# Kernel tuning notes

Measured on AMD Instinct MI355X. Metric: run time of the kernel, lower is better.

Reference implementation:

```python
import jax, jax.numpy as jnp
import numpy as np

N, E = 100000, 3200000
F_IN, HID, NCLS = 1433, 8, 7
H1, H2 = 8, 1
NEG_SLOPE = 0.2


def gat_layer(x, W, att_src, att_dst, bias, src, dst, heads, ch):
    n = x.shape[0]
    h = (x @ W).reshape(n, heads, ch)                      # [N,H,C]
    a_s = (h * att_src).sum(-1)                            # [N,H]
    a_d = (h * att_dst).sum(-1)                            # [N,H]
    e = a_s[src] + a_d[dst]                                # [Etot,H]
    e = jnp.where(e > 0, e, NEG_SLOPE * e)                 # leaky_relu(0.2)
    m = jax.ops.segment_max(e, dst, num_segments=n)        # per-dst max
    e = jnp.exp(e - m[dst])
    denom = jax.ops.segment_sum(e, dst, num_segments=n)
    alpha = e / (denom[dst] + 1e-16)                       # segment softmax
    msg = h[src] * alpha[:, :, None]                       # [Etot,H,C]
    out = jax.ops.segment_sum(msg, dst, num_segments=n)    # [N,H,C]
    return out.mean(axis=1) + bias                         # concat=False -> head mean


def setup_inputs() -> dict:
    key = jax.random.key(0)
    ks = jax.random.split(key, 10)
    x = jax.random.normal(ks[0], (N, F_IN), dtype=jnp.float32)
    edge_index = jax.random.randint(ks[1], (2, E), 0, N, dtype=jnp.int32)
    s = 0.1
    W1 = jax.random.normal(ks[2], (F_IN, H1 * HID), dtype=jnp.float32) * s
    att_src1 = jax.random.normal(ks[3], (H1, HID), dtype=jnp.float32) * s
    att_dst1 = jax.random.normal(ks[4], (H1, HID), dtype=jnp.float32) * s
    b1 = jnp.zeros((HID,), dtype=jnp.float32)
    W2 = jax.random.normal(ks[5], (HID, H2 * NCLS), dtype=jnp.float32) * s
    att_src2 = jax.random.normal(ks[6], (H2, NCLS), dtype=jnp.float32) * s
    att_dst2 = jax.random.normal(ks[7], (H2, NCLS), dtype=jnp.float32) * s
    b2 = jnp.zeros((NCLS,), dtype=jnp.float32)
    return {"x": x, "edge_index": edge_index, "W1": W1, "att_src1": att_src1,
            "att_dst1": att_dst1, "b1": b1, "W2": W2, "att_src2": att_src2,
            "att_dst2": att_dst2, "b2": b2}


def reference(x, edge_index, W1, att_src1, att_dst1, b1, W2, att_src2, att_dst2, b2):
    n = x.shape[0]
    loops = jnp.arange(n, dtype=edge_index.dtype)
    src = jnp.concatenate([edge_index[0], loops])  # PyG add_self_loops=True
    dst = jnp.concatenate([edge_index[1], loops])
    h = jax.nn.elu(gat_layer(x, W1, att_src1, att_dst1, b1, src, dst, H1, HID))
    out = gat_layer(h, W2, att_src2, att_dst2, b2, src, dst, H2, NCLS)
    return jax.nn.log_softmax(out, axis=-1)
```

## Files before the change

### kernel.cpp

```cpp
#include <hip/hip_runtime.h>

#define N_NODES 100000
#define E_EDGES 3200000
#define F_IN    1433
#define K_PAD   1472
#define NCH     98
#define KPH     64

typedef _Float16 f16x4 __attribute__((ext_vector_type(4)));
typedef _Float16 f16x8 __attribute__((ext_vector_type(8)));
typedef float    f32x4 __attribute__((ext_vector_type(4)));

__device__ __forceinline__ void gload_lds16(const void* g, void* l) {
    __builtin_amdgcn_global_load_lds(
        (const __attribute__((address_space(1))) unsigned int*)g,
        (__attribute__((address_space(3))) unsigned int*)l, 16, 0, 0);
}

__global__ void k_init(const float* __restrict__ w1, _Float16* __restrict__ w1t,
                       int* __restrict__ counts) {
    int i = blockIdx.x * 256 + threadIdx.x;
    if (i < N_NODES) counts[i] = 0;
    if (i < 64 * K_PAD) {
        int n = i / K_PAD, k = i - n * K_PAD;
        float v = (k < F_IN) ? w1[(size_t)k * 64 + n] : 0.f;
        w1t[i] = (_Float16)v;
    }
}

__global__ void k_hist(const int* __restrict__ dst, int* __restrict__ counts) {
    int idx = blockIdx.x * 256 + threadIdx.x;
    int4 d4 = ((const int4*)dst)[idx];
    atomicAdd(&counts[d4.x], 1);
    atomicAdd(&counts[d4.y], 1);
    atomicAdd(&counts[d4.z], 1);
    atomicAdd(&counts[d4.w], 1);
}

__global__ void k_scan_a(const int* __restrict__ counts, int* __restrict__ csum) {
    __shared__ int sh[256];
    int b = blockIdx.x, t = threadIdx.x;
    int s = 0;
    for (int j = 0; j < 4; ++j) {
        int idx = b * 1024 + j * 256 + t;
        if (idx < N_NODES) s += counts[idx];
    }
    sh[t] = s; __syncthreads();
    for (int off = 128; off > 0; off >>= 1) {
        if (t < off) sh[t] += sh[t + off];
        __syncthreads();
    }
    if (t == 0) csum[b] = sh[0];
}

__global__ void k_scan_b(int* __restrict__ csum) {
    __shared__ int sh[128];
    int t = threadIdx.x;
    int v = (t < NCH) ? csum[t] : 0;
    sh[t] = v; __syncthreads();
    for (int off = 1; off < 128; off <<= 1) {
        int u = (t >= off) ? sh[t - off] : 0;
        __syncthreads();
        sh[t] += u;
        __syncthreads();
    }
    if (t < NCH) csum[t] = sh[t] - v;
}

__global__ void k_scan_c(const int* __restrict__ counts, const int* __restrict__ csum,
                         int* __restrict__ offsets, int* __restrict__ cursor) {
    __shared__ int sh[256];
    int b = blockIdx.x, t = threadIdx.x;
    int base = b * 1024 + t * 4;
    int c0 = (base + 0 < N_NODES) ? counts[base + 0] : 0;
    int c1 = (base + 1 < N_NODES) ? counts[base + 1] : 0;
    int c2 = (base + 2 < N_NODES) ? counts[base + 2] : 0;
    int c3 = (base + 3 < N_NODES) ? counts[base + 3] : 0;
    int tot = c0 + c1 + c2 + c3;
    sh[t] = tot; __syncthreads();
    for (int off = 1; off < 256; off <<= 1) {
        int v = (t >= off) ? sh[t - off] : 0;
        __syncthreads();
        sh[t] += v;
        __syncthreads();
    }
    int excl = sh[t] - tot;
    int o = csum[b] + excl;
    if (base + 0 < N_NODES) { offsets[base + 0] = o;            cursor[base + 0] = o; }
    if (base + 1 < N_NODES) { int q = o + c0;      offsets[base + 1] = q; cursor[base + 1] = q; }
    if (base + 2 < N_NODES) { int q = o + c0 + c1; offsets[base + 2] = q; cursor[base + 2] = q; }
    if (base + 3 < N_NODES) { int q = o + c0 + c1 + c2; offsets[base + 3] = q; cursor[base + 3] = q; }
}

__global__ __launch_bounds__(256) void k_gemm_scat(const float* __restrict__ x,
                                                   const _Float16* __restrict__ w1t,
                                                   const float* __restrict__ att_src1,
                                                   const float* __restrict__ att_dst1,
                                                   _Float16* __restrict__ h1,
                                                   float* __restrict__ a_s1,
                                                   float* __restrict__ a_d1,
                                                   const int* __restrict__ src,
                                                   const int* __restrict__ dst,
                                                   int* __restrict__ cursor,
                                                   int* __restrict__ sorted_src) {
    __shared__ __align__(16) char AsB[2][64 * 256];
    __shared__ __align__(16) char BsB[2][64 * 128];
    const int tid = threadIdx.x;

    if (blockIdx.x & 1) {
        const int sid = blockIdx.x >> 1;
        for (int sweep = 0; sweep < 7; ++sweep) {
            #pragma unroll
            for (int rep = 0; rep < 2; ++rep) {
                int i4 = sid * 512 + rep * 256 + tid;
                if (i4 < E_EDGES / 4) {
                    int4 s4 = ((const int4*)src)[i4];
                    int4 d4 = ((const int4*)dst)[i4];
                    int p;
                    if ((d4.x >> 14) == sweep) { p = atomicAdd(&cursor[d4.x], 1); sorted_src[p] = s4.x; }
                    if ((d4.y >> 14) == sweep) { p = atomicAdd(&cursor[d4.y], 1); sorted_src[p] = s4.y; }
                    if ((d4.z >> 14) == sweep) { p = atomicAdd(&cursor[d4.z], 1); sorted_src[p] = s4.z; }
                    if ((d4.w >> 14) == sweep) { p = atomicAdd(&cursor[d4.w], 1); sorted_src[p] = s4.w; }
                }
            }
        }
        return;
    }

    const int gid  = blockIdx.x >> 1;
    const int lane = tid & 63;
    const int wave = tid >> 6;
    const int l16  = lane & 15;
    const int l4   = lane >> 4;
    const int brow0 = gid * 64;

    f32x4 acc[4] = {};

    auto stageA = [&](int buf, int ph) {
        #pragma unroll
        for (int j = 0; j < 4; ++j) {
            int p = j * 256 + tid;
            int row = p >> 4, q = p & 15;
            int qs = q ^ (row & 7);
            int grow = brow0 + row; if (grow > N_NODES - 1) grow = N_NODES - 1;
            const float* gp = x + (size_t)grow * F_IN + ph * KPH + qs * 4;
            gload_lds16(gp, AsB[buf] + j * 4096 + wave * 1024);
        }
    };
    auto stageB = [&](int buf, int ph) {
        #pragma unroll
        for (int j = 0; j < 2; ++j) {
            int p = j * 256 + tid;
            int col = p >> 3, c = p & 7;
            int cs = c ^ (col & 7);
            const _Float16* gp = w1t + (size_t)col * K_PAD + ph * KPH + cs * 8;
            gload_lds16(gp, BsB[buf] + j * 4096 + wave * 1024);
        }
    };
    auto stageTailA = [&](int buf) {
        for (int i = tid; i < 1024; i += 256) {
            int row = i >> 4, q = i & 15;
            int qs = q ^ (row & 7);
            int grow = brow0 + row; if (grow > N_NODES - 1) grow = N_NODES - 1;
            const float* gp = x + (size_t)grow * F_IN;
            float4 v;
            #pragma unroll
            for (int jj = 0; jj < 4; ++jj) {
                int k = 1408 + qs * 4 + jj;
                ((float*)&v)[jj] = (k < F_IN) ? gp[k] : 0.f;
            }
            *(float4*)(AsB[buf] + row * 256 + q * 16) = v;
        }
    };
    auto compute = [&](int buf) {
        const int rA = wave * 16 + l16;
        const char* Ab = AsB[buf] + rA * 256;
        const int r7 = rA & 7;
        #pragma unroll
        for (int st = 0; st < 4; ++st) {
            float4 af = *(const float4*)(Ab + ((((st << 2) + l4) ^ r7) << 4));
            f16x4 a = { (_Float16)af.x, (_Float16)af.y, (_Float16)af.z, (_Float16)af.w };
            #pragma unroll
            for (int t = 0; t < 4; ++t) {
                const int cB = t * 16 + l16;
                const int chunk = (st << 1) + (l4 >> 1);
                const int boff = cB * 128 + ((chunk ^ (cB & 7)) << 4) + ((l4 & 1) << 3);
                f16x4 b = *(const f16x4*)(BsB[buf] + boff);
                acc[t] = __builtin_amdgcn_mfma_f32_16x16x16f16(a, b, acc[t], 0, 0, 0);
            }
        }
    };

    stageA(0, 0); stageB(0, 0);
    stageA(1, 1); stageB(1, 1);
    for (int ph = 0; ph <= 20; ++ph) {
        asm volatile("s_waitcnt vmcnt(6)" ::: "memory");
        __builtin_amdgcn_sched_barrier(0);
        __builtin_amdgcn_s_barrier();
        compute(ph & 1);
        asm volatile("s_waitcnt lgkmcnt(0)" ::: "memory");
        __builtin_amdgcn_s_barrier();
        int nxt = ph + 2;
        if (nxt < 22)       { stageA(ph & 1, nxt); stageB(ph & 1, nxt); }
        else if (nxt == 22) { stageTailA(ph & 1);  stageB(ph & 1, 22);  }
    }
    asm volatile("s_waitcnt vmcnt(0) lgkmcnt(0)" ::: "memory");
    __builtin_amdgcn_sched_barrier(0);
    __builtin_amdgcn_s_barrier();
    compute(1);
    compute(0);

    const int wrow0 = brow0 + wave * 16;
    #pragma unroll
    for (int t = 0; t < 4; ++t) {
        const int head = t * 2 + (l16 >> 3);
        const int ch   = l16 & 7;
        const float asc = att_src1[head * 8 + ch];
        const float adc = att_dst1[head * 8 + ch];
        #pragma unroll
        for (int j = 0; j < 4; ++j) {
            int r = wrow0 + l4 * 4 + j;
            float ps = acc[t][j] * asc, pd = acc[t][j] * adc;
            ps += __shfl_xor(ps, 1); ps += __shfl_xor(ps, 2); ps += __shfl_xor(ps, 4);
            pd += __shfl_xor(pd, 1); pd += __shfl_xor(pd, 2); pd += __shfl_xor(pd, 4);
            if (r < N_NODES) {
                h1[(size_t)r * 64 + t * 16 + l16] = (_Float16)acc[t][j];
                if (ch == 0) {
                    a_s1[r * 8 + head] = ps;
                    a_d1[r * 8 + head] = pd;
                }
            }
        }
    }
}

__global__ __launch_bounds__(256) void k_agg1(
    const int* __restrict__ offsets, const int* __restrict__ counts,
    const int* __restrict__ sorted_src,
    const float* __restrict__ a_s1, const float* __restrict__ a_d1,
    const _Float16* __restrict__ h1, const float* __restrict__ b1,
    const float* __restrict__ w2, const float* __restrict__ att_src2,
    const float* __restrict__ att_dst2,
    _Float16* __restrict__ g, float* __restrict__ a_s2, float* __restrict__ a_d2) {
    const int lane = threadIdx.x & 63;
    const int wave = threadIdx.x >> 6;
    const int h    = lane & 7;
    const int es   = lane >> 3;
    const int n    = blockIdx.x * 4 + wave;
    const int start = offsets[n];
    const int cnt   = counts[n];
    const float adn = a_d1[n * 8 + h];
    float et = a_s1[n * 8 + h] + adn;
    const float e_self = et > 0.f ? et : 0.2f * et;

    float m = e_self, denom = 0.f;
    float acc[8] = {0.f,0.f,0.f,0.f,0.f,0.f,0.f,0.f};
    if (es == 0) {
        denom = 1.f;
        f16x8 hv0 = *(const f16x8*)(h1 + (size_t)n * 64 + h * 8);
        #pragma unroll
        for (int c = 0; c < 8; ++c) acc[c] = (float)hv0[c];
    }
    for (int i = es; i < cnt; i += 32) {
        const int i1 = i + 8, i2 = i + 16, i3 = i + 24;
        const bool b1v = i1 < cnt, b2v = i2 < cnt, b3v = i3 < cnt;
        int s0 = sorted_src[start + i];
        int s1 = sorted_src[start + (b1v ? i1 : i)];
        int s2 = sorted_src[start + (b2v ? i2 : i)];
        int s3 = sorted_src[start + (b3v ? i3 : i)];
        float a0 = a_s1[s0 * 8 + h];
        float a1 = a_s1[s1 * 8 + h];
        float a2 = a_s1[s2 * 8 + h];
        float a3 = a_s1[s3 * 8 + h];
        f16x8 v0 = *(const f16x8*)(h1 + (size_t)s0 * 64 + h * 8);
        f16x8 v1 = *(const f16x8*)(h1 + (size_t)s1 * 64 + h * 8);
        f16x8 v2 = *(const f16x8*)(h1 + (size_t)s2 * 64 + h * 8);
        f16x8 v3 = *(const f16x8*)(h1 + (size_t)s3 * 64 + h * 8);
        {
            float e = a0 + adn; e = e > 0.f ? e : 0.2f * e;
            if (e > m + 8.f) { float sc = __expf(m - e); denom *= sc;
                #pragma unroll
                for (int c = 0; c < 8; ++c) acc[c] *= sc; m = e; }
            float p = __expf(e - m); denom += p;
            #pragma unroll
            for (int c = 0; c < 8; ++c) acc[c] += p * (float)v0[c];
        }
        if (b1v) {
            float e = a1 + adn; e = e > 0.f ? e : 0.2f * e;
            if (e > m + 8.f) { float sc = __expf(m - e); denom *= sc;
                #pragma unroll
                for (int c = 0; c < 8; ++c) acc[c] *= sc; m = e; }
            float p = __expf(e - m); denom += p;
            #pragma unroll
            for (int c = 0; c < 8; ++c) acc[c] += p * (float)v1[c];
        }
        if (b2v) {
            float e = a2 + adn; e = e > 0.f ? e : 0.2f * e;
            if (e > m + 8.f) { float sc = __expf(m - e); denom *= sc;
                #pragma unroll
                for (int c = 0; c < 8; ++c) acc[c] *= sc; m = e; }
            float p = __expf(e - m); denom += p;
            #pragma unroll
            for (int c = 0; c < 8; ++c) acc[c] += p * (float)v2[c];
        }
        if (b3v) {
            float e = a3 + adn; e = e > 0.f ? e : 0.2f * e;
            if (e > m + 8.f) { float sc = __expf(m - e); denom *= sc;
                #pragma unroll
                for (int c = 0; c < 8; ++c) acc[c] *= sc; m = e; }
            float p = __expf(e - m); denom += p;
            #pragma unroll
            for (int c = 0; c < 8; ++c) acc[c] += p * (float)v3[c];
        }
    }
    #pragma unroll
    for (int d = 8; d < 64; d <<= 1) {
        float mo = __shfl_xor(m, d);
        float dn = __shfl_xor(denom, d);
        float mn = fmaxf(m, mo);
        float sa = __expf(m - mn), sb = __expf(mo - mn);
        denom = denom * sa + dn * sb;
        #pragma unroll
        for (int c = 0; c < 8; ++c) {
            float ao = __shfl_xor(acc[c], d);
            acc[c] = acc[c] * sa + ao * sb;
        }
        m = mn;
    }
    float inv = 1.f / (denom + 1e-16f);
    float hc[8];
    #pragma unroll
    for (int c = 0; c < 8; ++c) {
        float v = acc[c] * inv;
        v += __shfl_xor(v, 1);
        v += __shfl_xor(v, 2);
        v += __shfl_xor(v, 4);
        float o = 0.125f * v + b1[c];
        hc[c] = o > 0.f ? o : expm1f(o);
    }
    if (lane == 0) {
        float s2 = 0.f, d2 = 0.f;
        f16x8 gr;
        #pragma unroll
        for (int j = 0; j < 7; ++j) {
            float t = 0.f;
            #pragma unroll
            for (int c = 0; c < 8; ++c) t += hc[c] * w2[c * 7 + j];
            gr[j] = (_Float16)t;
            s2 += t * att_src2[j];
            d2 += t * att_dst2[j];
        }
        gr[7] = (_Float16)0.f;
        *(f16x8*)(g + (size_t)n * 8) = gr;
        a_s2[n] = s2;
        a_d2[n] = d2;
    }
}

__global__ __launch_bounds__(256) void k_agg2(
    const int* __restrict__ offsets, const int* __restrict__ counts,
    const int* __restrict__ sorted_src,
    const float* __restrict__ a_s2, const float* __restrict__ a_d2,
    const _Float16* __restrict__ g, const float* __restrict__ b2,
    float* __restrict__ outp) {
    const int tid  = threadIdx.x;
    const int lane = tid & 63;
    const int wave = tid >> 6;
    const int grp  = lane >> 3;
    const int s    = lane & 7;
    const int n    = blockIdx.x * 32 + wave * 8 + grp;
    const int start = offsets[n];
    const int cnt   = counts[n];
    const float adn = a_d2[n];
    float et = a_s2[n] + adn;
    const float e_self = et > 0.f ? et : 0.2f * et;

    float m = e_self, denom = 0.f;
    float acc[8] = {0.f,0.f,0.f,0.f,0.f,0.f,0.f,0.f};
    if (s == 0) {
        denom = 1.f;
        f16x8 gv0 = *(const f16x8*)(g + (size_t)n * 8);
        #pragma unroll
        for (int c = 0; c < 8; ++c) acc[c] = (float)gv0[c];
    }
    for (int i = s; i < cnt; i += 32) {
        const int i1 = i + 8, i2 = i + 16, i3 = i + 24;
        const bool b1v = i1 < cnt, b2v = i2 < cnt, b3v = i3 < cnt;
        int s0 = sorted_src[start + i];
        int s1 = sorted_src[start + (b1v ? i1 : i)];
        int s2 = sorted_src[start + (b2v ? i2 : i)];
        int s3 = sorted_src[start + (b3v ? i3 : i)];
        float a0 = a_s2[s0], a1 = a_s2[s1], a2 = a_s2[s2], a3 = a_s2[s3];
        f16x8 v0 = *(const f16x8*)(g + (size_t)s0 * 8);
        f16x8 v1 = *(const f16x8*)(g + (size_t)s1 * 8);
        f16x8 v2 = *(const f16x8*)(g + (size_t)s2 * 8);
        f16x8 v3 = *(const f16x8*)(g + (size_t)s3 * 8);
        {
            float e = a0 + adn; e = e > 0.f ? e : 0.2f * e;
            if (e > m + 8.f) { float sc = __expf(m - e); denom *= sc;
                #pragma unroll
                for (int c = 0; c < 8; ++c) acc[c] *= sc; m = e; }
            float p = __expf(e - m); denom += p;
            #pragma unroll
            for (int c = 0; c < 8; ++c) acc[c] += p * (float)v0[c];
        }
        if (b1v) {
            float e = a1 + adn; e = e > 0.f ? e : 0.2f * e;
            if (e > m + 8.f) { float sc = __expf(m - e); denom *= sc;
                #pragma unroll
                for (int c = 0; c < 8; ++c) acc[c] *= sc; m = e; }
            float p = __expf(e - m); denom += p;
            #pragma unroll
            for (int c = 0; c < 8; ++c) acc[c] += p * (float)v1[c];
        }
        if (b2v) {
            float e = a2 + adn; e = e > 0.f ? e : 0.2f * e;
            if (e > m + 8.f) { float sc = __expf(m - e); denom *= sc;
                #pragma unroll
                for (int c = 0; c < 8; ++c) acc[c] *= sc; m = e; }
            float p = __expf(e - m); denom += p;
            #pragma unroll
            for (int c = 0; c < 8; ++c) acc[c] += p * (float)v2[c];
        }
        if (b3v) {
            float e = a3 + adn; e = e > 0.f ? e : 0.2f * e;
            if (e > m + 8.f) { float sc = __expf(m - e); denom *= sc;
                #pragma unroll
                for (int c = 0; c < 8; ++c) acc[c] *= sc; m = e; }
            float p = __expf(e - m); denom += p;
            #pragma unroll
            for (int c = 0; c < 8; ++c) acc[c] += p * (float)v3[c];
        }
    }
    #pragma unroll
    for (int d = 1; d < 8; d <<= 1) {
        float mo = __shfl_xor(m, d, 8);
        float dn = __shfl_xor(denom, d, 8);
        float mn = fmaxf(m, mo);
        float sa = __expf(m - mn), sb = __expf(mo - mn);
        denom = denom * sa + dn * sb;
        #pragma unroll
        for (int c = 0; c < 8; ++c) {
            float ao = __shfl_xor(acc[c], d, 8);
            acc[c] = acc[c] * sa + ao * sb;
        }
        m = mn;
    }
    float inv = 1.f / (denom + 1e-16f);
    float o[7]; float mx = -1e30f;
    #pragma unroll
    for (int c = 0; c < 7; ++c) { o[c] = acc[c] * inv + b2[c]; mx = fmaxf(mx, o[c]); }
    float se = 0.f;
    #pragma unroll
    for (int c = 0; c < 7; ++c) se += __expf(o[c] - mx);
    float ls = mx + logf(se);
    if (s < 7) outp[n * 7 + s] = o[s] - ls;
}

extern "C" void kernel_launch(void* const* d_in, const int* in_sizes, int n_in,
                              void* d_out, int out_size, void* d_ws, size_t ws_size,
                              hipStream_t stream) {
    const float* x        = (const float*)d_in[0];
    const int*   ei       = (const int*)d_in[1];
    const float* W1       = (const float*)d_in[2];
    const float* att_src1 = (const float*)d_in[3];
    const float* att_dst1 = (const float*)d_in[4];
    const float* b1       = (const float*)d_in[5];
    const float* W2       = (const float*)d_in[6];
    const float* att_src2 = (const float*)d_in[7];
    const float* att_dst2 = (const float*)d_in[8];
    const float* b2       = (const float*)d_in[9];
    const int* src = ei;
    const int* dst = ei + E_EDGES;

    char* ws = (char*)d_ws;
    size_t off = 0;
    auto alloc = [&](size_t bytes) -> char* {
        char* p = ws + off;
        off = (off + bytes + 255) & ~(size_t)255;
        return p;
    };
    _Float16* h1         = (_Float16*)alloc((size_t)N_NODES * 64 * 2);
    float*    a_s1       = (float*)   alloc((size_t)N_NODES * 8 * 4);
    float*    a_d1       = (float*)   alloc((size_t)N_NODES * 8 * 4);
    _Float16* w1t        = (_Float16*)alloc((size_t)64 * K_PAD * 2);
    int*      counts     = (int*)     alloc((size_t)N_NODES * 4);
    int*      offsets    = (int*)     alloc((size_t)N_NODES * 4);
    int*      cursor     = (int*)     alloc((size_t)N_NODES * 4);
    int*      csum       = (int*)     alloc((size_t)NCH * 4);
    int*      sorted_src = (int*)     alloc((size_t)(E_EDGES + 32) * 4);
    _Float16* gbuf       = (_Float16*)alloc((size_t)N_NODES * 8 * 2);
    float*    a_s2       = (float*)   alloc((size_t)N_NODES * 4);
    float*    a_d2       = (float*)   alloc((size_t)N_NODES * 4);
    float*    outp       = (float*)d_out;

    hipLaunchKernelGGL(k_init,      dim3(391),   dim3(256), 0, stream, W1, w1t, counts);
    hipLaunchKernelGGL(k_hist,      dim3(3125),  dim3(256), 0, stream, dst, counts);
    hipLaunchKernelGGL(k_scan_a,    dim3(NCH),   dim3(256), 0, stream, counts, csum);
    hipLaunchKernelGGL(k_scan_b,    dim3(1),     dim3(128), 0, stream, csum);
    hipLaunchKernelGGL(k_scan_c,    dim3(NCH),   dim3(256), 0, stream, counts, csum, offsets, cursor);
    hipLaunchKernelGGL(k_gemm_scat, dim3(3126),  dim3(256), 0, stream,
                       x, w1t, att_src1, att_dst1, h1, a_s1, a_d1,
                       src, dst, cursor, sorted_src);
    hipLaunchKernelGGL(k_agg1,      dim3(25000), dim3(256), 0, stream, offsets, counts, sorted_src,
                       a_s1, a_d1, h1, b1, W2, att_src2, att_dst2, gbuf, a_s2, a_d2);
    hipLaunchKernelGGL(k_agg2,      dim3(3125),  dim3(256), 0, stream, offsets, counts, sorted_src,
                       a_s2, a_d2, gbuf, b2, outp);
}
```

Measured before the change: 535.1 us.

## Split scatter from GEMM and deepen GEMM pipeline to four K32 stages

The fused GEMM-plus-edge-scatter kernel becomes two separate kernels: a standalone atomic scatter, and a layer-1 GEMM with K tiles of 32 and a four-buffer global-to-LDS pipeline in place of two buffers of 64. Padding K to 1440 lets the special scalar tail-staging path go away. For the last tile, the x loads now run past the end of each row into the next one, which is safe only because the padded weights there are zero. The goal is more loads in flight and a simpler GEMM, at the cost of no longer overlapping the scatter with the GEMM, plus an extra launch.

```diff
diff --git a/kernel.cpp b/kernel.cpp
--- a/kernel.cpp
+++ b/kernel.cpp
@@ -3,9 +3,9 @@
 #define N_NODES 100000
 #define E_EDGES 3200000
 #define F_IN    1433
-#define K_PAD   1472
+#define K_PAD   1440
 #define NCH     98
-#define KPH     64
+#define KPH     32
 
 typedef _Float16 f16x4 __attribute__((ext_vector_type(4)));
 typedef _Float16 f16x8 __attribute__((ext_vector_type(8)));
@@ -92,99 +92,75 @@
     if (base + 3 < N_NODES) { int q = o + c0 + c1 + c2; offsets[base + 3] = q; cursor[base + 3] = q; }
 }
 
-__global__ __launch_bounds__(256) void k_gemm_scat(const float* __restrict__ x,
-                                                   const _Float16* __restrict__ w1t,
-                                                   const float* __restrict__ att_src1,
-                                                   const float* __restrict__ att_dst1,
-                                                   _Float16* __restrict__ h1,
-                                                   float* __restrict__ a_s1,
-                                                   float* __restrict__ a_d1,
-                                                   const int* __restrict__ src,
-                                                   const int* __restrict__ dst,
-                                                   int* __restrict__ cursor,
-                                                   int* __restrict__ sorted_src) {
-    __shared__ __align__(16) char AsB[2][64 * 256];
-    __shared__ __align__(16) char BsB[2][64 * 128];
+__global__ void k_scatter(const int* __restrict__ src, const int* __restrict__ dst,
+                          int* __restrict__ cursor, int* __restrict__ sorted_src) {
     const int tid = threadIdx.x;
-
-    if (blockIdx.x & 1) {
-        const int sid = blockIdx.x >> 1;
-        for (int sweep = 0; sweep < 7; ++sweep) {
-            #pragma unroll
-            for (int rep = 0; rep < 2; ++rep) {
-                int i4 = sid * 512 + rep * 256 + tid;
-                if (i4 < E_EDGES / 4) {
-                    int4 s4 = ((const int4*)src)[i4];
-                    int4 d4 = ((const int4*)dst)[i4];
-                    int p;
-                    if ((d4.x >> 14) == sweep) { p = atomicAdd(&cursor[d4.x], 1); sorted_src[p] = s4.x; }
-                    if ((d4.y >> 14) == sweep) { p = atomicAdd(&cursor[d4.y], 1); sorted_src[p] = s4.y; }
-                    if ((d4.z >> 14) == sweep) { p = atomicAdd(&cursor[d4.z], 1); sorted_src[p] = s4.z; }
-                    if ((d4.w >> 14) == sweep) { p = atomicAdd(&cursor[d4.w], 1); sorted_src[p] = s4.w; }
-                }
+    const int sid = blockIdx.x;
+    for (int sweep = 0; sweep < 7; ++sweep) {
+        #pragma unroll
+        for (int rep = 0; rep < 2; ++rep) {
+            int i4 = sid * 512 + rep * 256 + tid;
+            if (i4 < E_EDGES / 4) {
+                int4 s4 = ((const int4*)src)[i4];
+                int4 d4 = ((const int4*)dst)[i4];
+                int p;
+                if ((d4.x >> 14) == sweep) { p = atomicAdd(&cursor[d4.x], 1); sorted_src[p] = s4.x; }
+                if ((d4.y >> 14) == sweep) { p = atomicAdd(&cursor[d4.y], 1); sorted_src[p] = s4.y; }
+                if ((d4.z >> 14) == sweep) { p = atomicAdd(&cursor[d4.z], 1); sorted_src[p] = s4.z; }
+                if ((d4.w >> 14) == sweep) { p = atomicAdd(&cursor[d4.w], 1); sorted_src[p] = s4.w; }
             }
         }
-        return;
-    }
-
-    const int gid  = blockIdx.x >> 1;
+    }
+}
+
+__global__ __launch_bounds__(256) void k_gemm1(const float* __restrict__ x,
+                                               const _Float16* __restrict__ w1t,
+                                               const float* __restrict__ att_src1,
+                                               const float* __restrict__ att_dst1,
+                                               _Float16* __restrict__ h1,
+                                               float* __restrict__ a_s1,
+                                               float* __restrict__ a_d1) {
+    __shared__ __align__(16) char AsB[4][64 * 128];
+    __shared__ __align__(16) char BsB[4][64 * 64];
+    const int tid  = threadIdx.x;
     const int lane = tid & 63;
     const int wave = tid >> 6;
     const int l16  = lane & 15;
     const int l4   = lane >> 4;
-    const int brow0 = gid * 64;
+    const int brow0 = blockIdx.x * 64;
 
     f32x4 acc[4] = {};
 
     auto stageA = [&](int buf, int ph) {
         #pragma unroll
-        for (int j = 0; j < 4; ++j) {
+        for (int j = 0; j < 2; ++j) {
             int p = j * 256 + tid;
-            int row = p >> 4, q = p & 15;
+            int row = p >> 3, q = p & 7;
             int qs = q ^ (row & 7);
-            int grow = brow0 + row; if (grow > N_NODES - 1) grow = N_NODES - 1;
+            int grow = brow0 + row; if (grow >= N_NODES) grow = 0;
             const float* gp = x + (size_t)grow * F_IN + ph * KPH + qs * 4;
             gload_lds16(gp, AsB[buf] + j * 4096 + wave * 1024);
         }
     };
     auto stageB = [&](int buf, int ph) {
-        #pragma unroll
-        for (int j = 0; j < 2; ++j) {
-            int p = j * 256 + tid;
-            int col = p >> 3, c = p & 7;
-            int cs = c ^ (col & 7);
-            const _Float16* gp = w1t + (size_t)col * K_PAD + ph * KPH + cs * 8;
-            gload_lds16(gp, BsB[buf] + j * 4096 + wave * 1024);
-        }
-    };
-    auto stageTailA = [&](int buf) {
-        for (int i = tid; i < 1024; i += 256) {
-            int row = i >> 4, q = i & 15;
-            int qs = q ^ (row & 7);
-            int grow = brow0 + row; if (grow > N_NODES - 1) grow = N_NODES - 1;
-            const float* gp = x + (size_t)grow * F_IN;
-            float4 v;
-            #pragma unroll
-            for (int jj = 0; jj < 4; ++jj) {
-                int k = 1408 + qs * 4 + jj;
-                ((float*)&v)[jj] = (k < F_IN) ? gp[k] : 0.f;
-            }
-            *(float4*)(AsB[buf] + row * 256 + q * 16) = v;
-        }
+        int col = tid >> 2, c = tid & 3;
+        int cs = c ^ (col & 3);
+        const _Float16* gp = w1t + (size_t)col * K_PAD + ph * KPH + cs * 8;
+        gload_lds16(gp, BsB[buf] + wave * 1024);
     };
     auto compute = [&](int buf) {
         const int rA = wave * 16 + l16;
-        const char* Ab = AsB[buf] + rA * 256;
+        const char* Ab = AsB[buf] + rA * 128;
         const int r7 = rA & 7;
         #pragma unroll
-        for (int st = 0; st < 4; ++st) {
+        for (int st = 0; st < 2; ++st) {
             float4 af = *(const float4*)(Ab + ((((st << 2) + l4) ^ r7) << 4));
             f16x4 a = { (_Float16)af.x, (_Float16)af.y, (_Float16)af.z, (_Float16)af.w };
             #pragma unroll
             for (int t = 0; t < 4; ++t) {
                 const int cB = t * 16 + l16;
                 const int chunk = (st << 1) + (l4 >> 1);
-                const int boff = cB * 128 + ((chunk ^ (cB & 7)) << 4) + ((l4 & 1) << 3);
+                const int boff = cB * 64 + ((chunk ^ (cB & 3)) << 4) + ((l4 & 1) << 3);
                 f16x4 b = *(const f16x4*)(BsB[buf] + boff);
                 acc[t] = __builtin_amdgcn_mfma_f32_16x16x16f16(a, b, acc[t], 0, 0, 0);
             }
@@ -193,22 +169,29 @@
 
     stageA(0, 0); stageB(0, 0);
     stageA(1, 1); stageB(1, 1);
-    for (int ph = 0; ph <= 20; ++ph) {
-        asm volatile("s_waitcnt vmcnt(6)" ::: "memory");
+    stageA(2, 2); stageB(2, 2);
+    stageA(3, 3); stageB(3, 3);
+    for (int ph = 0; ph <= 41; ++ph) {
+        asm volatile("s_waitcnt vmcnt(9)" ::: "memory");
         __builtin_amdgcn_sched_barrier(0);
         __builtin_amdgcn_s_barrier();
-        compute(ph & 1);
+        compute(ph & 3);
         asm volatile("s_waitcnt lgkmcnt(0)" ::: "memory");
         __builtin_amdgcn_s_barrier();
-        int nxt = ph + 2;
-        if (nxt < 22)       { stageA(ph & 1, nxt); stageB(ph & 1, nxt); }
-        else if (nxt == 22) { stageTailA(ph & 1);  stageB(ph & 1, 22);  }
-    }
-    asm volatile("s_waitcnt vmcnt(0) lgkmcnt(0)" ::: "memory");
+        if (ph <= 40) { stageA(ph & 3, ph + 4); stageB(ph & 3, ph + 4); }
+    }
+    asm volatile("s_waitcnt vmcnt(6)" ::: "memory");
     __builtin_amdgcn_sched_barrier(0);
     __builtin_amdgcn_s_barrier();
-    compute(1);
-    compute(0);
+    compute(42 & 3);
+    asm volatile("s_waitcnt vmcnt(3)" ::: "memory");
+    __builtin_amdgcn_sched_barrier(0);
+    __builtin_amdgcn_s_barrier();
+    compute(43 & 3);
+    asm volatile("s_waitcnt vmcnt(0)" ::: "memory");
+    __builtin_amdgcn_sched_barrier(0);
+    __builtin_amdgcn_s_barrier();
+    compute(44 & 3);
 
     const int wrow0 = brow0 + wave * 16;
     #pragma unroll
@@ -494,16 +477,16 @@
     float*    a_d2       = (float*)   alloc((size_t)N_NODES * 4);
     float*    outp       = (float*)d_out;
 
-    hipLaunchKernelGGL(k_init,      dim3(391),   dim3(256), 0, stream, W1, w1t, counts);
-    hipLaunchKernelGGL(k_hist,      dim3(3125),  dim3(256), 0, stream, dst, counts);
-    hipLaunchKernelGGL(k_scan_a,    dim3(NCH),   dim3(256), 0, stream, counts, csum);
-    hipLaunchKernelGGL(k_scan_b,    dim3(1),     dim3(128), 0, stream, csum);
-    hipLaunchKernelGGL(k_scan_c,    dim3(NCH),   dim3(256), 0, stream, counts, csum, offsets, cursor);
-    hipLaunchKernelGGL(k_gemm_scat, dim3(3126),  dim3(256), 0, stream,
-                       x, w1t, att_src1, att_dst1, h1, a_s1, a_d1,
-                       src, dst, cursor, sorted_src);
-    hipLaunchKernelGGL(k_agg1,      dim3(25000), dim3(256), 0, stream, offsets, counts, sorted_src,
+    hipLaunchKernelGGL(k_init,    dim3(391),   dim3(256), 0, stream, W1, w1t, counts);
+    hipLaunchKernelGGL(k_hist,    dim3(3125),  dim3(256), 0, stream, dst, counts);
+    hipLaunchKernelGGL(k_scan_a,  dim3(NCH),   dim3(256), 0, stream, counts, csum);
+    hipLaunchKernelGGL(k_scan_b,  dim3(1),     dim3(128), 0, stream, csum);
+    hipLaunchKernelGGL(k_scan_c,  dim3(NCH),   dim3(256), 0, stream, counts, csum, offsets, cursor);
+    hipLaunchKernelGGL(k_scatter, dim3(1563),  dim3(256), 0, stream, src, dst, cursor, sorted_src);
+    hipLaunchKernelGGL(k_gemm1,   dim3(1563),  dim3(256), 0, stream, x, w1t, att_src1, att_dst1,
+                       h1, a_s1, a_d1);
+    hipLaunchKernelGGL(k_agg1,    dim3(25000), dim3(256), 0, stream, offsets, counts, sorted_src,
                        a_s1, a_d1, h1, b1, W2, att_src2, att_dst2, gbuf, a_s2, a_d2);
-    hipLaunchKernelGGL(k_agg2,      dim3(3125),  dim3(256), 0, stream, offsets, counts, sorted_src,
+    hipLaunchKernelGGL(k_agg2,    dim3(3125),  dim3(256), 0, stream, offsets, counts, sorted_src,
                        a_s2, a_d2, gbuf, b2, outp);
 }
```

Result: slower. 622.2 us (+16.3%).
